# Kernel optimization log

Hardware: AMD Instinct MI355X
Metric: run time of the kernel (lower is better)

Reference implementation:

```python
import jax, jax.numpy as jnp
import numpy as np

EPS = 1e-6      # torch F.pairwise_distance default eps (added to the difference)
MARGIN = 0.5


def setup_inputs() -> dict:
    key = jax.random.key(0)
    k1, k2 = jax.random.split(key)
    batch = jax.random.normal(k1, (8192, 1024), dtype=jnp.float32)
    positive = jax.random.normal(k2, (1024,), dtype=jnp.float32)
    return {"batch": batch, "positive": positive}


def _loss(batch, positive):
    n, d = batch.shape
    # torch pairwise_distance(x, y) = ||x - y + eps||_2, so
    # ||a - b + eps||^2 = ||a||^2 + ||b||^2 - 2 a.b + 2*eps*(sum(a) - sum(b)) + d*eps^2
    sq = jnp.sum(batch * batch, axis=-1)                 # [n]
    dots = batch @ batch.T                               # [n, n] GEMM
    sums = jnp.sum(batch, axis=-1)                       # [n]
    d2 = (sq[:, None] + sq[None, :] - 2.0 * dots
          + 2.0 * EPS * (sums[:, None] - sums[None, :]) + d * EPS * EPS)
    # exclude self (the python loop concatenates batch[:i], batch[i+1:])
    neg_inf = jnp.asarray(-jnp.inf, d2.dtype)
    d2_masked = jnp.where(jnp.eye(n, dtype=bool), neg_inf, d2)
    max_neg = jnp.sqrt(jnp.maximum(jnp.max(d2_masked, axis=-1), 0.0))  # [n]
    # distance anchor -> positive (with torch eps convention)
    diff = batch - positive[None, :] + EPS
    pos_dist = jnp.sqrt(jnp.sum(diff * diff, axis=-1))   # [n]
    losses = jax.nn.relu(pos_dist - max_neg + MARGIN)    # [n]
    # anchors exactly equal to the positive are skipped in the original loop
    valid = ~jnp.all(batch == positive[None, :], axis=-1)
    cnt = jnp.sum(valid.astype(losses.dtype))
    return jnp.sum(jnp.where(valid, losses, 0.0)) / cnt


def reference(batch, positive):
    return _loss(batch, positive)
```

## Files before the change

### kernel.cpp

```cpp
#include <hip/hip_runtime.h>
#include <hip/hip_bf16.h>


#define NROWS 8192
#define DIM   1024
#define BTM   256
#define BTN   128
#define BK    32
#define NKT   (DIM / BK)
#define NUNITS 1056

constexpr float EPS = 1e-6f;
constexpr float MARGIN = 0.5f;

typedef __attribute__((ext_vector_type(8))) short short8;
typedef __attribute__((ext_vector_type(4))) float f32x4;

__device__ __forceinline__ unsigned short f2bf_rne(float f) {
    unsigned u = __float_as_uint(f);
    u += 0x7fffu + ((u >> 16) & 1u);
    return (unsigned short)(u >> 16);
}

__global__ void prep_kernel(const float* __restrict__ X, const float* __restrict__ P,
                            unsigned short* __restrict__ Xb,
                            float* __restrict__ cj, float* __restrict__ basei,
                            float* __restrict__ posd, int* __restrict__ valid)
{
    const int tid  = threadIdx.x;
    const int w    = tid >> 6;
    const int lane = tid & 63;
    const int row  = blockIdx.x * 4 + w;
    const float* xr = X + (size_t)row * DIM;

    float sq = 0.f, sm = 0.f, pd = 0.f;
    bool eq = true;
    #pragma unroll
    for (int it = 0; it < 4; ++it) {
        const int idx = it * 256 + lane * 4;
        const float4 x = *(const float4*)(xr + idx);
        const float4 p = *(const float4*)(P + idx);
        sq += x.x*x.x + x.y*x.y + x.z*x.z + x.w*x.w;
        sm += x.x + x.y + x.z + x.w;
        const float d0 = x.x - p.x + EPS, d1 = x.y - p.y + EPS;
        const float d2 = x.z - p.z + EPS, d3 = x.w - p.w + EPS;
        pd += d0*d0 + d1*d1 + d2*d2 + d3*d3;
        eq = eq && (x.x == p.x) && (x.y == p.y) && (x.z == p.z) && (x.w == p.w);
        ushort4 b;
        b.x = f2bf_rne(x.x); b.y = f2bf_rne(x.y); b.z = f2bf_rne(x.z); b.w = f2bf_rne(x.w);
        *(ushort4*)(Xb + (size_t)row * DIM + idx) = b;
    }
    #pragma unroll
    for (int off = 32; off >= 1; off >>= 1) {
        sq += __shfl_xor(sq, off);
        sm += __shfl_xor(sm, off);
        pd += __shfl_xor(pd, off);
    }
    const bool alleq = __all(eq);
    if (lane == 0) {
        cj[row]    = sq - 2.f * EPS * sm;
        basei[row] = sq + 2.f * EPS * sm + (float)DIM * EPS * EPS;
        posd[row]  = sqrtf(pd);
        valid[row] = alleq ? 0 : 1;
    }
}

__global__ __launch_bounds__(512, 4) void gemm_max_kernel(
        const unsigned short* __restrict__ Xb,
        const float* __restrict__ cj,
        float* __restrict__ partmax)
{
    __shared__ alignas(16) unsigned short lds[2][1536 * 8];

    const int tid  = threadIdx.x;
    const int lane = tid & 63;
    const int wid  = tid >> 6;
    const int wm   = wid >> 1;
    const int wn   = wid & 1;
    const int l15  = lane & 15;
    const int lk   = lane >> 4;
    const int cx   = lk ^ ((l15 >> 1) & 3);

    const int t0 = (blockIdx.x & 7) * (NUNITS / 8) + (blockIdx.x >> 3);
    int bm = (int)(32.5f - sqrtf(1056.25f - (float)t0));
    if (bm < 0) bm = 0;
    if (bm > 31) bm = 31;
    while (bm > 0 && 65 * bm - bm * bm > t0) --bm;
    while (65 * (bm + 1) - (bm + 1) * (bm + 1) <= t0) ++bm;
    const int bn = 2 * bm + (t0 - (65 * bm - bm * bm));
    const int Mbase = bm * BTM, Nbase = bn * BTN;

    f32x4 acc[4][4];
    #pragma unroll
    for (int m = 0; m < 4; ++m)
        #pragma unroll
        for (int n = 0; n < 4; ++n)
            acc[m][n] = (f32x4){0.f, 0.f, 0.f, 0.f};

    #define STAGE(BUF, KT) do {                                                               \
        _Pragma("unroll")                                                                     \
        for (int inst_ = 0; inst_ < 2; ++inst_) {                                             \
            const int q_ = inst_ * 512 + tid;                                                 \
            const int r_ = q_ >> 2;                                                           \
            const int c_ = (q_ & 3) ^ ((q_ >> 3) & 3);                                        \
            const unsigned short* src_ = Xb + (size_t)(Mbase + r_) * DIM + (KT) * BK + c_ * 8; \
            unsigned short* dst_ = &lds[BUF][(inst_ * 512 + wid * 64) * 8];                   \
            __builtin_amdgcn_global_load_lds((const __attribute__((address_space(1))) void*)src_, \
                                             (__attribute__((address_space(3))) void*)dst_, 16, 0, 0); \
        }                                                                                     \
        {                                                                                     \
            const int r_ = tid >> 2;                                                          \
            const int c_ = (tid & 3) ^ ((tid >> 3) & 3);                                      \
            const unsigned short* src_ = Xb + (size_t)(Nbase + r_) * DIM + (KT) * BK + c_ * 8; \
            unsigned short* dst_ = &lds[BUF][(1024 + wid * 64) * 8];                          \
            __builtin_amdgcn_global_load_lds((const __attribute__((address_space(1))) void*)src_, \
                                             (__attribute__((address_space(3))) void*)dst_, 16, 0, 0); \
        }                                                                                     \
    } while (0)

    STAGE(0, 0);
    __syncthreads();

    #pragma unroll 2
    for (int kt = 0; kt < NKT; ++kt) {
        const int b = kt & 1;
        if (kt + 1 < NKT) STAGE(b ^ 1, kt + 1);

        const unsigned short* Ab = &lds[b][0];
        const unsigned short* Bb = &lds[b][1024 * 8];
        short8 af[4], bf[4];
        #pragma unroll
        for (int mt = 0; mt < 4; ++mt)
            af[mt] = *(const short8*)(Ab + (((wm * 64 + mt * 16 + l15) << 2) + cx) * 8);
        #pragma unroll
        for (int nt = 0; nt < 4; ++nt)
            bf[nt] = *(const short8*)(Bb + (((wn * 64 + nt * 16 + l15) << 2) + cx) * 8);

        __builtin_amdgcn_s_setprio(1);
        #pragma unroll
        for (int mt = 0; mt < 4; ++mt)
            #pragma unroll
            for (int nt = 0; nt < 4; ++nt)
                acc[mt][nt] = __builtin_amdgcn_mfma_f32_16x16x32_bf16(af[mt], bf[nt], acc[mt][nt], 0, 0, 0);
        __builtin_amdgcn_s_setprio(0);

        __syncthreads();
    }
    #undef STAGE

    float* scratchf = (float*)&lds[0][0];
    float cv[4];
    #pragma unroll
    for (int n = 0; n < 4; ++n)
        cv[n] = cj[Nbase + wn * 64 + n * 16 + l15];

    float vt[4];
    #pragma unroll
    for (int n = 0; n < 4; ++n) vt[n] = -__builtin_inff();

    #pragma unroll
    for (int m = 0; m < 4; ++m) {
        #pragma unroll
        for (int r = 0; r < 4; ++r) {
            const int lrow = wm * 64 + m * 16 + lk * 4 + r;
            const int grow = Mbase + lrow;
            const float ci = cj[grow];
            float rv = -__builtin_inff();
            #pragma unroll
            for (int n = 0; n < 4; ++n) {
                const float dot2 = 2.f * acc[m][n][r];
                const bool dg = (grow == Nbase + wn * 64 + n * 16 + l15);
                float vr = cv[n] - dot2;
                float vc = ci - dot2;
                if (dg) { vr = -__builtin_inff(); vc = -__builtin_inff(); }
                rv = fmaxf(rv, vr);
                vt[n] = fmaxf(vt[n], vc);
            }
            #pragma unroll
            for (int off = 8; off >= 1; off >>= 1)
                rv = fmaxf(rv, __shfl_xor(rv, off));
            if (l15 == 0) scratchf[wn * 256 + lrow] = rv;
        }
    }
    #pragma unroll
    for (int n = 0; n < 4; ++n) {
        vt[n] = fmaxf(vt[n], __shfl_xor(vt[n], 16));
        vt[n] = fmaxf(vt[n], __shfl_xor(vt[n], 32));
        if (lk == 0) scratchf[512 + wm * 128 + wn * 64 + n * 16 + l15] = vt[n];
    }
    __syncthreads();

    if (tid < BTM) {
        partmax[(size_t)bn * NROWS + Mbase + tid] = fmaxf(scratchf[tid], scratchf[256 + tid]);
    } else if (tid < BTM + BTN) {
        const int c = tid - BTM;
        const float v = fmaxf(fmaxf(scratchf[512 + c], scratchf[640 + c]),
                              fmaxf(scratchf[768 + c], scratchf[896 + c]));
        partmax[(size_t)(64 + bm) * NROWS + Nbase + c] = v;
    }
}

__global__ void finalize1_kernel(const float* __restrict__ partmax,
                                 const float* __restrict__ basei,
                                 const float* __restrict__ posd,
                                 const int* __restrict__ valid,
                                 float* __restrict__ partials)
{
    const int tid = threadIdx.x;
    const int a   = blockIdx.x;
    const int row = a * 256 + tid;
    float m = -__builtin_inff();
    for (int bn = 2 * a; bn < 64; ++bn)
        m = fmaxf(m, partmax[(size_t)bn * NROWS + row]);
    for (int bm2 = 0; bm2 <= a; ++bm2)
        m = fmaxf(m, partmax[(size_t)(64 + bm2) * NROWS + row]);
    const float d2 = m + basei[row];
    const float mn = sqrtf(fmaxf(d2, 0.f));
    float loss = fmaxf(posd[row] - mn + MARGIN, 0.f);
    float cnt = 1.f;
    if (!valid[row]) { loss = 0.f; cnt = 0.f; }
    #pragma unroll
    for (int off = 32; off >= 1; off >>= 1) {
        loss += __shfl_xor(loss, off);
        cnt  += __shfl_xor(cnt, off);
    }
    __shared__ float sl[4], sc[4];
    const int w = tid >> 6, lane = tid & 63;
    if (lane == 0) { sl[w] = loss; sc[w] = cnt; }
    __syncthreads();
    if (tid == 0) {
        partials[blockIdx.x * 2]     = sl[0] + sl[1] + sl[2] + sl[3];
        partials[blockIdx.x * 2 + 1] = sc[0] + sc[1] + sc[2] + sc[3];
    }
}

__global__ void finalize2_kernel(const float* __restrict__ partials, float* __restrict__ out)
{
    const int tid = threadIdx.x;
    float l = 0.f, c = 0.f;
    if (tid < 32) { l = partials[tid * 2]; c = partials[tid * 2 + 1]; }
    #pragma unroll
    for (int off = 32; off >= 1; off >>= 1) {
        l += __shfl_xor(l, off);
        c += __shfl_xor(c, off);
    }
    if (tid == 0) out[0] = l / c;
}

extern "C" void kernel_launch(void* const* d_in, const int* in_sizes, int n_in,
                              void* d_out, int out_size, void* d_ws, size_t ws_size,
                              hipStream_t stream)
{
    const float* X = (const float*)d_in[0];
    const float* P = (const float*)d_in[1];
    float* out = (float*)d_out;
    char* ws = (char*)d_ws;

    unsigned short* Xb = (unsigned short*)ws;
    size_t off = (size_t)NROWS * DIM * sizeof(unsigned short);
    float* cj    = (float*)(ws + off);  off += (size_t)NROWS * 4;
    float* basei = (float*)(ws + off);  off += (size_t)NROWS * 4;
    float* posd  = (float*)(ws + off);  off += (size_t)NROWS * 4;
    int*   valid = (int*)(ws + off);    off += (size_t)NROWS * 4;
    float* partmax = (float*)(ws + off); off += (size_t)96 * NROWS * 4;
    float* partials = (float*)(ws + off);

    prep_kernel<<<NROWS / 4, 256, 0, stream>>>(X, P, Xb, cj, basei, posd, valid);
    gemm_max_kernel<<<NUNITS, 512, 0, stream>>>(Xb, cj, partmax);
    finalize1_kernel<<<NROWS / 256, 256, 0, stream>>>(partmax, basei, posd, valid, partials);
    finalize2_kernel<<<1, 64, 0, stream>>>(partials, out);
}
```

Before: 118.5 us.

## Halve GEMM block to 4 waves with 128x64 per-wave tiles

The GEMM-max kernel now runs 256 threads (4 waves) per block instead of 512. Each wave computes a 128x64 output tile with 32 accumulators instead of a 64x64 tile. Each wave reuses its B fragments across two A sub-tiles, which raises MFMA work per LDS read and cuts barrier participants. The cost is higher register pressure and lower occupancy (launch bounds 256,2), leaving fewer waves to hide memory latency.

```diff
diff --git a/kernel.cpp b/kernel.cpp
--- a/kernel.cpp
+++ b/kernel.cpp
@@ -65,7 +65,7 @@
     }
 }
 
-__global__ __launch_bounds__(512, 4) void gemm_max_kernel(
+__global__ __launch_bounds__(256, 2) void gemm_max_kernel(
         const unsigned short* __restrict__ Xb,
         const float* __restrict__ cj,
         float* __restrict__ partmax)
@@ -90,29 +90,31 @@
     const int bn = 2 * bm + (t0 - (65 * bm - bm * bm));
     const int Mbase = bm * BTM, Nbase = bn * BTN;
 
-    f32x4 acc[4][4];
-    #pragma unroll
-    for (int m = 0; m < 4; ++m)
+    f32x4 acc[8][4];
+    #pragma unroll
+    for (int m = 0; m < 8; ++m)
         #pragma unroll
         for (int n = 0; n < 4; ++n)
             acc[m][n] = (f32x4){0.f, 0.f, 0.f, 0.f};
 
     #define STAGE(BUF, KT) do {                                                               \
         _Pragma("unroll")                                                                     \
-        for (int inst_ = 0; inst_ < 2; ++inst_) {                                             \
-            const int q_ = inst_ * 512 + tid;                                                 \
+        for (int inst_ = 0; inst_ < 4; ++inst_) {                                             \
+            const int q_ = inst_ * 256 + tid;                                                 \
             const int r_ = q_ >> 2;                                                           \
             const int c_ = (q_ & 3) ^ ((q_ >> 3) & 3);                                        \
             const unsigned short* src_ = Xb + (size_t)(Mbase + r_) * DIM + (KT) * BK + c_ * 8; \
-            unsigned short* dst_ = &lds[BUF][(inst_ * 512 + wid * 64) * 8];                   \
+            unsigned short* dst_ = &lds[BUF][(inst_ * 256 + wid * 64) * 8];                   \
             __builtin_amdgcn_global_load_lds((const __attribute__((address_space(1))) void*)src_, \
                                              (__attribute__((address_space(3))) void*)dst_, 16, 0, 0); \
         }                                                                                     \
-        {                                                                                     \
-            const int r_ = tid >> 2;                                                          \
-            const int c_ = (tid & 3) ^ ((tid >> 3) & 3);                                      \
+        _Pragma("unroll")                                                                     \
+        for (int inst_ = 0; inst_ < 2; ++inst_) {                                             \
+            const int q_ = inst_ * 256 + tid;                                                 \
+            const int r_ = q_ >> 2;                                                           \
+            const int c_ = (q_ & 3) ^ ((q_ >> 3) & 3);                                        \
             const unsigned short* src_ = Xb + (size_t)(Nbase + r_) * DIM + (KT) * BK + c_ * 8; \
-            unsigned short* dst_ = &lds[BUF][(1024 + wid * 64) * 8];                          \
+            unsigned short* dst_ = &lds[BUF][(1024 + inst_ * 256 + wid * 64) * 8];            \
             __builtin_amdgcn_global_load_lds((const __attribute__((address_space(1))) void*)src_, \
                                              (__attribute__((address_space(3))) void*)dst_, 16, 0, 0); \
         }                                                                                     \
@@ -128,10 +130,11 @@
 
         const unsigned short* Ab = &lds[b][0];
         const unsigned short* Bb = &lds[b][1024 * 8];
-        short8 af[4], bf[4];
-        #pragma unroll
-        for (int mt = 0; mt < 4; ++mt)
-            af[mt] = *(const short8*)(Ab + (((wm * 64 + mt * 16 + l15) << 2) + cx) * 8);
+        short8 af[4], af2[4], bf[4];
+
+        #pragma unroll
+        for (int mt = 0; mt < 4; ++mt)
+            af[mt] = *(const short8*)(Ab + (((wm * 128 + mt * 16 + l15) << 2) + cx) * 8);
         #pragma unroll
         for (int nt = 0; nt < 4; ++nt)
             bf[nt] = *(const short8*)(Bb + (((wn * 64 + nt * 16 + l15) << 2) + cx) * 8);
@@ -144,6 +147,18 @@
                 acc[mt][nt] = __builtin_amdgcn_mfma_f32_16x16x32_bf16(af[mt], bf[nt], acc[mt][nt], 0, 0, 0);
         __builtin_amdgcn_s_setprio(0);
 
+        #pragma unroll
+        for (int mt = 0; mt < 4; ++mt)
+            af2[mt] = *(const short8*)(Ab + (((wm * 128 + 64 + mt * 16 + l15) << 2) + cx) * 8);
+
+        __builtin_amdgcn_s_setprio(1);
+        #pragma unroll
+        for (int mt = 0; mt < 4; ++mt)
+            #pragma unroll
+            for (int nt = 0; nt < 4; ++nt)
+                acc[4 + mt][nt] = __builtin_amdgcn_mfma_f32_16x16x32_bf16(af2[mt], bf[nt], acc[4 + mt][nt], 0, 0, 0);
+        __builtin_amdgcn_s_setprio(0);
+
         __syncthreads();
     }
     #undef STAGE
@@ -159,10 +174,10 @@
     for (int n = 0; n < 4; ++n) vt[n] = -__builtin_inff();
 
     #pragma unroll
-    for (int m = 0; m < 4; ++m) {
+    for (int m = 0; m < 8; ++m) {
         #pragma unroll
         for (int r = 0; r < 4; ++r) {
-            const int lrow = wm * 64 + m * 16 + lk * 4 + r;
+            const int lrow = wm * 128 + m * 16 + lk * 4 + r;
             const int grow = Mbase + lrow;
             const float ci = cj[grow];
             float rv = -__builtin_inff();
@@ -190,14 +205,9 @@
     }
     __syncthreads();
 
-    if (tid < BTM) {
-        partmax[(size_t)bn * NROWS + Mbase + tid] = fmaxf(scratchf[tid], scratchf[256 + tid]);
-    } else if (tid < BTM + BTN) {
-        const int c = tid - BTM;
-        const float v = fmaxf(fmaxf(scratchf[512 + c], scratchf[640 + c]),
-                              fmaxf(scratchf[768 + c], scratchf[896 + c]));
-        partmax[(size_t)(64 + bm) * NROWS + Nbase + c] = v;
-    }
+    partmax[(size_t)bn * NROWS + Mbase + tid] = fmaxf(scratchf[tid], scratchf[256 + tid]);
+    if (tid < BTN)
+        partmax[(size_t)(64 + bm) * NROWS + Nbase + tid] = fmaxf(scratchf[512 + tid], scratchf[640 + tid]);
 }
 
 __global__ void finalize1_kernel(const float* __restrict__ partmax,
@@ -266,7 +276,7 @@
     float* partials = (float*)(ws + off);
 
     prep_kernel<<<NROWS / 4, 256, 0, stream>>>(X, P, Xb, cj, basei, posd, valid);
-    gemm_max_kernel<<<NUNITS, 512, 0, stream>>>(Xb, cj, partmax);
+    gemm_max_kernel<<<NUNITS, 256, 0, stream>>>(Xb, cj, partmax);
     finalize1_kernel<<<NROWS / 256, 256, 0, stream>>>(partmax, basei, posd, valid, partials);
     finalize2_kernel<<<1, 64, 0, stream>>>(partials, out);
 }
```

After: 126.7 us. 6.9% more time.
